# Optimization experiments

Measured on AMD Instinct MI355X. Metric: run time of the kernel, lower is better.

## Reference

```python
import jax, jax.numpy as jnp
import numpy as np

A_CUBIC = -0.5  # Keys cubic-convolution parameter (order-3 spline approximation)


def _cubic(t):
    # Keys cubic interpolation kernel, support (-2, 2)
    at = jnp.abs(t)
    at2 = at * at
    at3 = at2 * at
    a = A_CUBIC
    w_inner = (a + 2.0) * at3 - (a + 3.0) * at2 + 1.0          # |t| <= 1
    w_outer = a * at3 - 5.0 * a * at2 + 8.0 * a * at - 4.0 * a  # 1 < |t| < 2
    return jnp.where(at <= 1.0, w_inner, jnp.where(at < 2.0, w_outer, 0.0))


def _spline_upsample_matrix(n_out, n_ctrl):
    # (n_out, n_ctrl) dense weight matrix interpolating control points to the
    # full-resolution axis with the cubic kernel; edge taps clamped (nearest).
    u = jnp.arange(n_out, dtype=jnp.float32) * (n_ctrl - 1) / (n_out - 1)
    i0 = jnp.floor(u).astype(jnp.int32)
    taps = i0[:, None] + jnp.arange(-1, 3)                      # (n_out, 4)
    w = _cubic(u[:, None] - taps.astype(jnp.float32))           # (n_out, 4)
    taps_c = jnp.clip(taps, 0, n_ctrl - 1)
    B = jnp.zeros((n_out, n_ctrl), jnp.float32)
    B = B.at[jnp.arange(n_out)[:, None], taps_c].add(w)
    return B


def _elastic_warp(img, displacement):
    # img: (H, W, C); displacement: (2, 3, 3) control-point displacements (dy, dx)
    H, W, C = img.shape
    By = _spline_upsample_matrix(H, displacement.shape[1])      # (H, 3)
    Bx = _spline_upsample_matrix(W, displacement.shape[2])      # (W, 3)
    disp = jnp.einsum('hy,dyx,wx->dhw', By, displacement, Bx)   # (2, H, W)

    yy = jnp.arange(H, dtype=jnp.float32)[:, None] + disp[0]    # sample coords
    xx = jnp.arange(W, dtype=jnp.float32)[None, :] + disp[1]
    iy0 = jnp.floor(yy).astype(jnp.int32)
    ix0 = jnp.floor(xx).astype(jnp.int32)

    out = jnp.zeros_like(img)
    # 4x4 cubic tap stencil (fixed small loop; each iteration is one full gather)
    for a in range(-1, 3):
        ty = iy0 + a
        wy = _cubic(yy - ty.astype(jnp.float32))                # (H, W)
        tyc = jnp.clip(ty, 0, H - 1)
        for b in range(-1, 3):
            tx = ix0 + b
            wx = _cubic(xx - tx.astype(jnp.float32))            # (H, W)
            txc = jnp.clip(tx, 0, W - 1)
            out = out + (wy * wx)[..., None] * img[tyc, txc]    # gather (H,W,C)
    return out


def setup_inputs() -> dict:
    key = jax.random.key(0)
    k1, k2 = jax.random.split(key)
    H, W, C = 2048, 4096, 3
    inputs = jax.random.normal(k1, (H, W, C), dtype=jnp.float32)
    displacement = jax.random.normal(k2, (2, 3, 3), dtype=jnp.float32)
    return {"inputs": inputs, "displacement": displacement}


def reference(inputs, displacement):
    # module draws displacement ~ N(0,1)*5 internally; externalized here
    return _elastic_warp(inputs, displacement * 5.0)
```

## Files before the change

kernel.cpp:

```cpp
#include <hip/hip_runtime.h>
#include <math.h>

constexpr int H = 2048;
constexpr int W = 4096;

__device__ __forceinline__ float k_inner(float t) {
    return fmaf(fmaf(1.5f, t, -2.5f), t * t, 1.0f);
}
__device__ __forceinline__ float k_outer(float t) {
    return fmaf(fmaf(fmaf(-0.5f, t, 2.5f), t, -4.0f), t, 2.0f);
}
__device__ __forceinline__ float cubic_w(float t) {
    float at = fabsf(t);
    if (at <= 1.0f) return k_inner(at);
    if (at < 2.0f)  return k_outer(at);
    return 0.0f;
}

__global__ __launch_bounds__(256)
void elastic_warp_kernel(const float* __restrict__ img,
                         const float* __restrict__ dctrl,
                         float* __restrict__ out) {
    int h = blockIdx.x >> 4;
    int w = ((blockIdx.x & 15) << 8) | threadIdx.x;

    __shared__ float s_cy[6];
    if (threadIdx.x == 0) {
        float u = (float)(2 * h) / (float)(H - 1);
        float i0 = floorf(u);
        float by0 = 0.0f, by1 = 0.0f, by2 = 0.0f;
#pragma unroll
        for (int k = -1; k < 3; ++k) {
            float tap = i0 + (float)k;
            float wt = cubic_w(u - tap);
            int tc = (int)tap;
            tc = tc < 0 ? 0 : (tc > 2 ? 2 : tc);
            if (tc == 0) by0 += wt; else if (tc == 1) by1 += wt; else by2 += wt;
        }
#pragma unroll
        for (int x = 0; x < 3; ++x) {
            s_cy[x]     = 5.0f * (by0 * dctrl[x] + by1 * dctrl[3 + x] + by2 * dctrl[6 + x]);
            s_cy[3 + x] = 5.0f * (by0 * dctrl[9 + x] + by1 * dctrl[12 + x] + by2 * dctrl[15 + x]);
        }
    }
    __syncthreads();

    float u = (float)(2 * w) / (float)(W - 1);
    bool hi = u >= 1.0f;
    float s = u - (hi ? 1.0f : 0.0f);
    float o1 = k_outer(1.0f + s);
    float is = k_inner(s);
    float i1 = k_inner(1.0f - s);
    float o2 = k_outer(2.0f - s);
    float bx0 = hi ? o1 : (o1 + is);
    float bx1 = hi ? is : i1;
    float bx2 = hi ? (i1 + o2) : o2;

    float d0 = s_cy[0] * bx0 + s_cy[1] * bx1 + s_cy[2] * bx2;
    float d1 = s_cy[3] * bx0 + s_cy[4] * bx1 + s_cy[5] * bx2;

    float yy = (float)h + d0;
    float xx = (float)w + d1;
    float iy0f = floorf(yy);
    float ix0f = floorf(xx);
    float fy = yy - iy0f;
    float fx = xx - ix0f;
    int iy0 = (int)iy0f;
    int ix0 = (int)ix0f;

    float wy0 = k_outer(1.0f + fy), wy1 = k_inner(fy), wy2 = k_inner(1.0f - fy), wy3 = k_outer(2.0f - fy);
    float wx0 = k_outer(1.0f + fx), wx1 = k_inner(fx), wx2 = k_inner(1.0f - fx), wx3 = k_outer(2.0f - fx);
    float wy[4] = {wy0, wy1, wy2, wy3};

    float acc0 = 0.0f, acc1 = 0.0f, acc2 = 0.0f;

    bool interior = (iy0 >= 1) & (iy0 <= H - 3) & (ix0 >= 1) & (ix0 <= W - 3);
    if (interior) {
        const float* base = img + ((size_t)(iy0 - 1) * W + (size_t)(ix0 - 1)) * 3;
#pragma unroll
        for (int a = 0; a < 4; ++a) {
            const float4* p4 = (const float4*)(base + (size_t)a * (W * 3));
            float4 v0 = p4[0];
            float4 v1 = p4[1];
            float4 v2 = p4[2];
            float ay = wy[a];
            float w0 = ay * wx0, w1 = ay * wx1, w2 = ay * wx2, w3 = ay * wx3;
            acc0 += w0 * v0.x + w1 * v0.w + w2 * v1.z + w3 * v2.y;
            acc1 += w0 * v0.y + w1 * v1.x + w2 * v1.w + w3 * v2.z;
            acc2 += w0 * v0.z + w1 * v1.y + w2 * v2.x + w3 * v2.w;
        }
    } else {
        float wx[4] = {wx0, wx1, wx2, wx3};
#pragma unroll
        for (int a = 0; a < 4; ++a) {
            int ty = iy0 + a - 1;
            ty = ty < 0 ? 0 : (ty > H - 1 ? H - 1 : ty);
            const float* row = img + (size_t)ty * (W * 3);
            float ay = wy[a];
#pragma unroll
            for (int b = 0; b < 4; ++b) {
                int tx = ix0 + b - 1;
                tx = tx < 0 ? 0 : (tx > W - 1 ? W - 1 : tx);
                float wgt = ay * wx[b];
                const float* p = row + tx * 3;
                acc0 += wgt * p[0];
                acc1 += wgt * p[1];
                acc2 += wgt * p[2];
            }
        }
    }

    float* o = out + ((size_t)h * W + (size_t)w) * 3;
    o[0] = acc0;
    o[1] = acc1;
    o[2] = acc2;
}

extern "C" void kernel_launch(void* const* d_in, const int* in_sizes, int n_in,
                              void* d_out, int out_size, void* d_ws, size_t ws_size,
                              hipStream_t stream) {
    const float* img   = (const float*)d_in[0];
    const float* dctrl = (const float*)d_in[1];
    float* out = (float*)d_out;

    int blocks = (H * W) / 256;
    elastic_warp_kernel<<<blocks, 256, 0, stream>>>(img, dctrl, out);
}
```

Baseline: 67.75 us.

## Compute two output rows per thread sharing overlapping stencil row loads

Each thread now produces two vertically adjacent output pixels. When their integer sample positions differ by exactly one row and share the same column, it loads five source rows instead of eight and reuses three of them between the two stencils. Otherwise it falls back to the clamped scalar path for both pixels. The grid is halved and per-thread register pressure rises, and the fast path only applies when the displacement field varies slowly between rows.

```diff
diff --git a/kernel.cpp b/kernel.cpp
--- a/kernel.cpp
+++ b/kernel.cpp
@@ -3,6 +3,7 @@
 
 constexpr int H = 2048;
 constexpr int W = 4096;
+constexpr int RS = W * 3;
 
 __device__ __forceinline__ float k_inner(float t) {
     return fmaf(fmaf(1.5f, t, -2.5f), t * t, 1.0f);
@@ -17,15 +18,21 @@
     return 0.0f;
 }
 
+#define ROWACC(va, vb, vc, q0, q1, q2, q3, A0, A1, A2)                              \
+    A0 = fmaf(q0, va.x, fmaf(q1, va.w, fmaf(q2, vb.z, fmaf(q3, vc.y, A0))));        \
+    A1 = fmaf(q0, va.y, fmaf(q1, vb.x, fmaf(q2, vb.w, fmaf(q3, vc.z, A1))));        \
+    A2 = fmaf(q0, va.z, fmaf(q1, vb.y, fmaf(q2, vc.x, fmaf(q3, vc.w, A2))));
+
 __global__ __launch_bounds__(256)
 void elastic_warp_kernel(const float* __restrict__ img,
                          const float* __restrict__ dctrl,
                          float* __restrict__ out) {
-    int h = blockIdx.x >> 4;
-    int w = ((blockIdx.x & 15) << 8) | threadIdx.x;
+    int h0 = (blockIdx.x >> 4) * 2;
+    int w  = ((blockIdx.x & 15) << 8) | threadIdx.x;
 
-    __shared__ float s_cy[6];
-    if (threadIdx.x == 0) {
+    __shared__ float s_cy[12];
+    if (threadIdx.x < 2) {
+        int h = h0 + (int)threadIdx.x;
         float u = (float)(2 * h) / (float)(H - 1);
         float i0 = floorf(u);
         float by0 = 0.0f, by1 = 0.0f, by2 = 0.0f;
@@ -37,83 +44,121 @@
             tc = tc < 0 ? 0 : (tc > 2 ? 2 : tc);
             if (tc == 0) by0 += wt; else if (tc == 1) by1 += wt; else by2 += wt;
         }
+        float* cy = s_cy + threadIdx.x * 6;
 #pragma unroll
         for (int x = 0; x < 3; ++x) {
-            s_cy[x]     = 5.0f * (by0 * dctrl[x] + by1 * dctrl[3 + x] + by2 * dctrl[6 + x]);
-            s_cy[3 + x] = 5.0f * (by0 * dctrl[9 + x] + by1 * dctrl[12 + x] + by2 * dctrl[15 + x]);
+            cy[x]     = 5.0f * (by0 * dctrl[x]     + by1 * dctrl[3 + x]  + by2 * dctrl[6 + x]);
+            cy[3 + x] = 5.0f * (by0 * dctrl[9 + x] + by1 * dctrl[12 + x] + by2 * dctrl[15 + x]);
         }
     }
     __syncthreads();
 
-    float u = (float)(2 * w) / (float)(W - 1);
-    bool hi = u >= 1.0f;
-    float s = u - (hi ? 1.0f : 0.0f);
+    float u = (float)w * (2.0f / 4095.0f);
+    bool hiu = u >= 1.0f;
+    float s = u - (hiu ? 1.0f : 0.0f);
     float o1 = k_outer(1.0f + s);
     float is = k_inner(s);
     float i1 = k_inner(1.0f - s);
     float o2 = k_outer(2.0f - s);
-    float bx0 = hi ? o1 : (o1 + is);
-    float bx1 = hi ? is : i1;
-    float bx2 = hi ? (i1 + o2) : o2;
+    float bx0 = hiu ? o1 : (o1 + is);
+    float bx1 = hiu ? is : i1;
+    float bx2 = hiu ? (i1 + o2) : o2;
 
-    float d0 = s_cy[0] * bx0 + s_cy[1] * bx1 + s_cy[2] * bx2;
-    float d1 = s_cy[3] * bx0 + s_cy[4] * bx1 + s_cy[5] * bx2;
+    float d0a = s_cy[0] * bx0 + s_cy[1] * bx1 + s_cy[2]  * bx2;
+    float d1a = s_cy[3] * bx0 + s_cy[4] * bx1 + s_cy[5]  * bx2;
+    float d0b = s_cy[6] * bx0 + s_cy[7] * bx1 + s_cy[8]  * bx2;
+    float d1b = s_cy[9] * bx0 + s_cy[10] * bx1 + s_cy[11] * bx2;
 
-    float yy = (float)h + d0;
-    float xx = (float)w + d1;
-    float iy0f = floorf(yy);
-    float ix0f = floorf(xx);
-    float fy = yy - iy0f;
-    float fx = xx - ix0f;
-    int iy0 = (int)iy0f;
-    int ix0 = (int)ix0f;
+    float yy0 = (float)h0 + d0a,        xx0 = (float)w + d1a;
+    float yy1 = (float)(h0 + 1) + d0b,  xx1 = (float)w + d1b;
+    float fl_y0 = floorf(yy0), fl_x0 = floorf(xx0);
+    float fl_y1 = floorf(yy1), fl_x1 = floorf(xx1);
+    float fy0 = yy0 - fl_y0, fx0 = xx0 - fl_x0;
+    float fy1 = yy1 - fl_y1, fx1 = xx1 - fl_x1;
+    int iy0 = (int)fl_y0, ix0 = (int)fl_x0;
+    int iy1 = (int)fl_y1, ix1 = (int)fl_x1;
 
-    float wy0 = k_outer(1.0f + fy), wy1 = k_inner(fy), wy2 = k_inner(1.0f - fy), wy3 = k_outer(2.0f - fy);
-    float wx0 = k_outer(1.0f + fx), wx1 = k_inner(fx), wx2 = k_inner(1.0f - fx), wx3 = k_outer(2.0f - fx);
-    float wy[4] = {wy0, wy1, wy2, wy3};
+    float wy0[4] = {k_outer(1.0f + fy0), k_inner(fy0), k_inner(1.0f - fy0), k_outer(2.0f - fy0)};
+    float wy1[4] = {k_outer(1.0f + fy1), k_inner(fy1), k_inner(1.0f - fy1), k_outer(2.0f - fy1)};
+    float wxa[4] = {k_outer(1.0f + fx0), k_inner(fx0), k_inner(1.0f - fx0), k_outer(2.0f - fx0)};
+    float wxb[4] = {k_outer(1.0f + fx1), k_inner(fx1), k_inner(1.0f - fx1), k_outer(2.0f - fx1)};
 
-    float acc0 = 0.0f, acc1 = 0.0f, acc2 = 0.0f;
+    float a0 = 0.f, a1 = 0.f, a2 = 0.f;
+    float b0 = 0.f, b1 = 0.f, b2 = 0.f;
 
-    bool interior = (iy0 >= 1) & (iy0 <= H - 3) & (ix0 >= 1) & (ix0 <= W - 3);
-    if (interior) {
-        const float* base = img + ((size_t)(iy0 - 1) * W + (size_t)(ix0 - 1)) * 3;
-#pragma unroll
-        for (int a = 0; a < 4; ++a) {
-            const float4* p4 = (const float4*)(base + (size_t)a * (W * 3));
-            float4 v0 = p4[0];
-            float4 v1 = p4[1];
-            float4 v2 = p4[2];
-            float ay = wy[a];
-            float w0 = ay * wx0, w1 = ay * wx1, w2 = ay * wx2, w3 = ay * wx3;
-            acc0 += w0 * v0.x + w1 * v0.w + w2 * v1.z + w3 * v2.y;
-            acc1 += w0 * v0.y + w1 * v1.x + w2 * v1.w + w3 * v2.z;
-            acc2 += w0 * v0.z + w1 * v1.y + w2 * v2.x + w3 * v2.w;
-        }
+    bool fast = (iy1 == iy0 + 1) & (ix1 == ix0) &
+                (iy0 >= 1) & (iy0 <= H - 4) & (ix0 >= 1) & (ix0 <= W - 3);
+
+    if (fast) {
+        int off = ((iy0 - 1) * W + (ix0 - 1)) * 3;
+        const float* base = img + off;
+        const float4* r0 = (const float4*)(base);
+        const float4* r1 = (const float4*)(base + RS);
+        const float4* r2 = (const float4*)(base + 2 * RS);
+        const float4* r3 = (const float4*)(base + 3 * RS);
+        const float4* r4 = (const float4*)(base + 4 * RS);
+        float4 v0a = r0[0], v0b = r0[1], v0c = r0[2];
+        float4 v1a = r1[0], v1b = r1[1], v1c = r1[2];
+        float4 v2a = r2[0], v2b = r2[1], v2c = r2[2];
+        float4 v3a = r3[0], v3b = r3[1], v3c = r3[2];
+        float4 v4a = r4[0], v4b = r4[1], v4c = r4[2];
+
+        { float q0=wy0[0]*wxa[0], q1=wy0[0]*wxa[1], q2=wy0[0]*wxa[2], q3=wy0[0]*wxa[3];
+          ROWACC(v0a, v0b, v0c, q0, q1, q2, q3, a0, a1, a2) }
+        { float q0=wy0[1]*wxa[0], q1=wy0[1]*wxa[1], q2=wy0[1]*wxa[2], q3=wy0[1]*wxa[3];
+          ROWACC(v1a, v1b, v1c, q0, q1, q2, q3, a0, a1, a2) }
+        { float q0=wy0[2]*wxa[0], q1=wy0[2]*wxa[1], q2=wy0[2]*wxa[2], q3=wy0[2]*wxa[3];
+          ROWACC(v2a, v2b, v2c, q0, q1, q2, q3, a0, a1, a2) }
+        { float q0=wy0[3]*wxa[0], q1=wy0[3]*wxa[1], q2=wy0[3]*wxa[2], q3=wy0[3]*wxa[3];
+          ROWACC(v3a, v3b, v3c, q0, q1, q2, q3, a0, a1, a2) }
+        { float q0=wy1[0]*wxb[0], q1=wy1[0]*wxb[1], q2=wy1[0]*wxb[2], q3=wy1[0]*wxb[3];
+          ROWACC(v1a, v1b, v1c, q0, q1, q2, q3, b0, b1, b2) }
+        { float q0=wy1[1]*wxb[0], q1=wy1[1]*wxb[1], q2=wy1[1]*wxb[2], q3=wy1[1]*wxb[3];
+          ROWACC(v2a, v2b, v2c, q0, q1, q2, q3, b0, b1, b2) }
+        { float q0=wy1[2]*wxb[0], q1=wy1[2]*wxb[1], q2=wy1[2]*wxb[2], q3=wy1[2]*wxb[3];
+          ROWACC(v3a, v3b, v3c, q0, q1, q2, q3, b0, b1, b2) }
+        { float q0=wy1[3]*wxb[0], q1=wy1[3]*wxb[1], q2=wy1[3]*wxb[2], q3=wy1[3]*wxb[3];
+          ROWACC(v4a, v4b, v4c, q0, q1, q2, q3, b0, b1, b2) }
     } else {
-        float wx[4] = {wx0, wx1, wx2, wx3};
 #pragma unroll
         for (int a = 0; a < 4; ++a) {
             int ty = iy0 + a - 1;
             ty = ty < 0 ? 0 : (ty > H - 1 ? H - 1 : ty);
-            const float* row = img + (size_t)ty * (W * 3);
-            float ay = wy[a];
+            int rowoff = ty * RS;
+            float ay = wy0[a];
 #pragma unroll
             for (int b = 0; b < 4; ++b) {
                 int tx = ix0 + b - 1;
                 tx = tx < 0 ? 0 : (tx > W - 1 ? W - 1 : tx);
-                float wgt = ay * wx[b];
-                const float* p = row + tx * 3;
-                acc0 += wgt * p[0];
-                acc1 += wgt * p[1];
-                acc2 += wgt * p[2];
+                float wgt = ay * wxa[b];
+                const float* p = img + rowoff + tx * 3;
+                a0 += wgt * p[0]; a1 += wgt * p[1]; a2 += wgt * p[2];
+            }
+        }
+#pragma unroll
+        for (int a = 0; a < 4; ++a) {
+            int ty = iy1 + a - 1;
+            ty = ty < 0 ? 0 : (ty > H - 1 ? H - 1 : ty);
+            int rowoff = ty * RS;
+            float ay = wy1[a];
+#pragma unroll
+            for (int b = 0; b < 4; ++b) {
+                int tx = ix1 + b - 1;
+                tx = tx < 0 ? 0 : (tx > W - 1 ? W - 1 : tx);
+                float wgt = ay * wxb[b];
+                const float* p = img + rowoff + tx * 3;
+                b0 += wgt * p[0]; b1 += wgt * p[1]; b2 += wgt * p[2];
             }
         }
     }
 
-    float* o = out + ((size_t)h * W + (size_t)w) * 3;
-    o[0] = acc0;
-    o[1] = acc1;
-    o[2] = acc2;
+    int o0 = (h0 * W + w) * 3;
+    out[o0]          = a0;
+    out[o0 + 1]      = a1;
+    out[o0 + 2]      = a2;
+    out[o0 + RS]     = b0;
+    out[o0 + RS + 1] = b1;
+    out[o0 + RS + 2] = b2;
 }
 
 extern "C" void kernel_launch(void* const* d_in, const int* in_sizes, int n_in,
@@ -123,6 +168,6 @@
     const float* dctrl = (const float*)d_in[1];
     float* out = (float*)d_out;
 
-    int blocks = (H * W) / 256;
+    int blocks = (H / 2) * (W / 256);
     elastic_warp_kernel<<<blocks, 256, 0, stream>>>(img, dctrl, out);
 }
```

Measured after the change: 70.23 us. +3.7%, slower.
